# Performance work log

Measured on AMD Instinct MI355X. Metric: run time of the kernel, lower is better.

The kernel has to match this reference:

```python
import jax, jax.numpy as jnp
import numpy as np

BN_EPS = 1e-5


def _gcn(x, A, W, gamma, beta):
    # x: [B,N,Cin], A: [B,N,N] -> [B,N,Cout]; BatchNorm1d over (B,N) per channel (train-mode batch stats)
    h = jnp.einsum('bnm,bmc->bnc', A, x @ W)
    mu = h.mean(axis=(0, 1))
    var = h.var(axis=(0, 1))
    h = (h - mu) * jax.lax.rsqrt(var + BN_EPS) * gamma + beta
    return jax.nn.relu(h)  # dropout is identity (drop_prob=0 / eval)


def _ppige(x, A, W0, g0, b0, W_res, g_res, b_res):
    h = _gcn(x, A, W0, g0, b0)
    for i in range(W_res.shape[0]):  # residual GCN stack (num_GCN-1 layers)
        h = _gcn(h, A, W_res[i], g_res[i], b_res[i]) + h
    return h


def _gge(x, w1, b1, w2, b2):
    return jax.nn.relu(jax.nn.relu(x @ w1 + b1) @ w2 + b2)


def _gaga(G, h):
    # G: [B,N,H], h: [B,H]
    att = jax.nn.softmax(jnp.einsum('bnh,bh->bn', G, h), axis=-1)
    return jnp.einsum('bnh,bn->bh', G, att)


def _led(ea, eb, conv_w, conv_b, p1_w, p1_b, p2_w, p2_b):
    # ea, eb: [B, 2H]; Conv1d(2H->2H, k=1) over length-2 axis then MaxPool1d(2)
    stacked = jnp.stack([ea, eb], axis=-1)  # [B, 2H, 2]
    conv = jnp.einsum('oc,bct->bot', conv_w, stacked) + conv_b[None, :, None]
    cnn_x = conv.max(axis=-1)  # [B, 2H]
    x = jax.nn.relu(jnp.concatenate([cnn_x, ea - eb], axis=1) @ p1_w + p1_b)
    return x @ p2_w + p2_b


def setup_inputs() -> dict:
    key = jax.random.key(0)
    ks = jax.random.split(key, 24)
    Bs, N, PPI_in, H, F_in = 8, 2048, 512, 256, 1024
    n_res = 3  # num_GCN - 1
    s = 0.02
    adjA = jax.random.uniform(ks[0], (Bs, N, N), jnp.float32)
    adjB = jax.random.uniform(ks[1], (Bs, N, N), jnp.float32)
    adjA = adjA / adjA.sum(-1, keepdims=True)  # row-normalized for numerical sanity
    adjB = adjB / adjB.sum(-1, keepdims=True)
    return {
        'a': jax.random.normal(ks[2], (Bs, F_in), jnp.float32),
        'bio_a': jax.random.normal(ks[3], (Bs, N, PPI_in), jnp.float32),
        'A': adjA,
        'b': jax.random.normal(ks[4], (Bs, F_in), jnp.float32),
        'bio_b': jax.random.normal(ks[5], (Bs, N, PPI_in), jnp.float32),
        'B': adjB,
        'W0': jax.random.normal(ks[6], (PPI_in, H), jnp.float32) * s,
        'gamma0': jnp.ones((H,), jnp.float32),
        'beta0': jnp.zeros((H,), jnp.float32),
        'W_res': jax.random.normal(ks[7], (n_res, H, H), jnp.float32) * s,
        'gamma_res': jnp.ones((n_res, H), jnp.float32),
        'beta_res': jnp.zeros((n_res, H), jnp.float32),
        'g1_w': jax.random.normal(ks[8], (F_in, 128), jnp.float32) * s,
        'g1_b': jnp.zeros((128,), jnp.float32),
        'g2_w': jax.random.normal(ks[9], (128, H), jnp.float32) * s,
        'g2_b': jnp.zeros((H,), jnp.float32),
        'conv_w': jax.random.normal(ks[10], (2 * H, 2 * H), jnp.float32) * s,
        'conv_b': jnp.zeros((2 * H,), jnp.float32),
        'p1_w': jax.random.normal(ks[11], (4 * H, H), jnp.float32) * s,
        'p1_b': jnp.zeros((H,), jnp.float32),
        'p2_w': jax.random.normal(ks[12], (H, 2), jnp.float32) * s,
        'p2_b': jnp.zeros((2,), jnp.float32),
    }


def reference(a, bio_a, A, b, bio_b, B, W0, gamma0, beta0, W_res, gamma_res, beta_res,
              g1_w, g1_b, g2_w, g2_b, conv_w, conv_b, p1_w, p1_b, p2_w, p2_b):
    Ga = _ppige(bio_a, A, W0, gamma0, beta0, W_res, gamma_res, beta_res)
    Gb = _ppige(bio_b, B, W0, gamma0, beta0, W_res, gamma_res, beta_res)
    ha = _gge(a, g1_w, g1_b, g2_w, g2_b)
    hb = _gge(b, g1_w, g1_b, g2_w, g2_b)
    ea = jnp.concatenate([ha, _gaga(Ga, ha)], axis=-1)
    eb = jnp.concatenate([hb, _gaga(Gb, hb)], axis=-1)
    logits = _led(ea, eb, conv_w, conv_b, p1_w, p1_b, p2_w, p2_b)
    return jax.nn.log_softmax(logits, axis=-1)
```

## Files before the change

### kernel.cpp

```cpp
#include <hip/hip_runtime.h>
#include <hip/hip_bf16.h>
#include <cstdint>

typedef unsigned short u16;
typedef __bf16 bf16x8 __attribute__((ext_vector_type(8)));
typedef float f32x4 __attribute__((ext_vector_type(4)));

typedef __attribute__((address_space(1))) const void* gas_ptr;
typedef __attribute__((address_space(3))) void* las_ptr;

__device__ __forceinline__ u16 f2bf(float f) {
  union { __hip_bfloat16 h; u16 u; } v;
  v.h = __float2bfloat16(f);
  return v.u;
}

__device__ __forceinline__ void gload16(const u16* g, u16* l) {
  __builtin_amdgcn_global_load_lds((gas_ptr)g, (las_ptr)l, 16, 0, 0);
}

__global__ __launch_bounds__(256) void k_convert_all(const float* __restrict__ aA,
                                                     const float* __restrict__ aB,
                                                     const float* __restrict__ bA,
                                                     const float* __restrict__ bB,
                                                     u16* __restrict__ Abf,
                                                     u16* __restrict__ biobf) {
  long i4 = (long)blockIdx.x * 256 + threadIdx.x;
  for (; i4 < 20971520L; i4 += (long)gridDim.x * 256) {
    const float* src; u16* dst; long off;
    if (i4 < 8388608L)        { src = aA; dst = Abf;              off = i4; }
    else if (i4 < 16777216L)  { src = aB; dst = Abf + 33554432L;  off = i4 - 8388608L; }
    else if (i4 < 18874368L)  { src = bA; dst = biobf;            off = i4 - 16777216L; }
    else                      { src = bB; dst = biobf + 8388608L; off = i4 - 18874368L; }
    float4 v = reinterpret_cast<const float4*>(src)[off];
    ushort4 o;
    o.x = f2bf(v.x); o.y = f2bf(v.y); o.z = f2bf(v.z); o.w = f2bf(v.w);
    reinterpret_cast<ushort4*>(dst)[off] = o;
  }
}

__global__ __launch_bounds__(256) void k_transpose_bf16(const float* __restrict__ src,
                                                        u16* __restrict__ dst, int R, int C) {
  __shared__ float tile[32][33];
  int c0 = blockIdx.x * 32, r0 = blockIdx.y * 32;
  int tx = threadIdx.x & 31, ty = threadIdx.x >> 5;
#pragma unroll
  for (int i = 0; i < 4; ++i) {
    int r = ty + i * 8;
    tile[r][tx] = src[(long)(r0 + r) * C + c0 + tx];
  }
  __syncthreads();
#pragma unroll
  for (int i = 0; i < 4; ++i) {
    int c = ty + i * 8;
    dst[(long)(c0 + c) * R + r0 + tx] = f2bf(tile[tx][c]);
  }
}

template<int EPI>
__global__ __launch_bounds__(256) void k_gemm(const u16* __restrict__ A, int lda, long sA,
                                              const u16* __restrict__ Bt, int ldb, long sB,
                                              float* __restrict__ C, int ldc, long sC,
                                              u16* __restrict__ PtOut, int ldpt,
                                              float* __restrict__ stats, int K) {
  __shared__ __align__(16) u16 smem[4][8192];
  __shared__ float cs[256];
  const int tid = threadIdx.x;
  const int lane = tid & 63;
  const int wid = tid >> 6;
  const int wm = wid >> 1, wn = wid & 1;
  const long m0 = (long)blockIdx.x * 128, n0 = (long)blockIdx.y * 128;
  const int z = blockIdx.z;
  const u16* Ab = A + (long)z * sA;
  const u16* Btb = Bt + (long)z * sB;

  const int rsub = lane >> 3;
  const int swzcol = ((lane & 7) ^ rsub) * 8;
  const long a_row = m0 + wid * 32 + rsub;
  const long b_row = n0 + wid * 32 + rsub;

  if (EPI == 0) cs[tid] = 0.f;

  const f32x4 zero = {0.f, 0.f, 0.f, 0.f};
  f32x4 acc[4][4];
#pragma unroll
  for (int i = 0; i < 4; ++i)
#pragma unroll
    for (int j = 0; j < 4; ++j) acc[i][j] = zero;

  const int fr = lane & 15;
  const int kgrp = lane >> 4;
  const int swz_rd = lane & 7;
  const int nk = K >> 6;

  auto stage = [&](int buf, int k0) {
#pragma unroll
    for (int i = 0; i < 4; ++i)
      gload16(Ab + (a_row + i * 8) * lda + (k0 + swzcol), &smem[buf][(wid * 32 + i * 8) * 64]);
#pragma unroll
    for (int i = 0; i < 4; ++i)
      gload16(Btb + (b_row + i * 8) * ldb + (k0 + swzcol), &smem[2 + buf][(wid * 32 + i * 8) * 64]);
  };

  stage(0, 0);
  __syncthreads();
  for (int t = 0; t < nk; ++t) {
    int cur = t & 1;
    if (t + 1 < nk) stage(1 - cur, (t + 1) * 64);
    const u16* Asb = smem[cur];
    const u16* Bsb = smem[2 + cur];
#pragma unroll
    for (int ks = 0; ks < 2; ++ks) {
      bf16x8 af[4], bfv[4];
#pragma unroll
      for (int f = 0; f < 4; ++f) {
        int cA = (ks * 4 + kgrp) ^ swz_rd;
        af[f]  = *reinterpret_cast<const bf16x8*>(&Asb[(wm * 64 + f * 16 + fr) * 64 + cA * 8]);
        bfv[f] = *reinterpret_cast<const bf16x8*>(&Bsb[(wn * 64 + f * 16 + fr) * 64 + cA * 8]);
      }
#pragma unroll
      for (int mf = 0; mf < 4; ++mf)
#pragma unroll
        for (int nf = 0; nf < 4; ++nf)
          acc[mf][nf] = __builtin_amdgcn_mfma_f32_16x16x32_bf16(af[mf], bfv[nf], acc[mf][nf], 0, 0, 0);
    }
    __syncthreads();
  }

  if (EPI == 0) {
    float* Cb = C + (long)z * sC;
    const int side = z >> 3;
#pragma unroll
    for (int mf = 0; mf < 4; ++mf) {
      long mrow = m0 + wm * 64 + mf * 16 + kgrp * 4;
#pragma unroll
      for (int nf = 0; nf < 4; ++nf) {
        long ncol = n0 + wn * 64 + nf * 16 + fr;
#pragma unroll
        for (int r = 0; r < 4; ++r)
          Cb[(mrow + r) * ldc + ncol] = acc[mf][nf][r];
      }
    }
#pragma unroll
    for (int nf = 0; nf < 4; ++nf) {
      int cl = wn * 64 + nf * 16 + fr;
      float s = 0.f, q = 0.f;
#pragma unroll
      for (int mf = 0; mf < 4; ++mf)
#pragma unroll
        for (int r = 0; r < 4; ++r) { float v = acc[mf][nf][r]; s += v; q += v * v; }
      atomicAdd(&cs[cl], s);
      atomicAdd(&cs[128 + cl], q);
    }
    __syncthreads();
    if (tid < 128) atomicAdd(&stats[side * 512 + n0 + tid], cs[tid]);
    else           atomicAdd(&stats[side * 512 + 256 + n0 + (tid - 128)], cs[tid]);
  } else {
    u16* Ts = &smem[0][0];
#pragma unroll
    for (int mf = 0; mf < 4; ++mf)
#pragma unroll
      for (int nf = 0; nf < 4; ++nf) {
        int nl = wn * 64 + nf * 16 + fr;
        int ml = wm * 64 + mf * 16 + kgrp * 4;
#pragma unroll
        for (int r = 0; r < 4; ++r)
          Ts[nl * 136 + ml + r] = f2bf(acc[mf][nf][r]);
      }
    __syncthreads();
    int n = tid >> 1, half = tid & 1;
    const u16* sp = Ts + n * 136 + half * 64;
    u16* dp = PtOut + (long)(n0 + n) * ldpt + m0 + half * 64;
#pragma unroll
    for (int j = 0; j < 8; ++j)
      reinterpret_cast<uint4*>(dp)[j] = reinterpret_cast<const uint4*>(sp)[j];
  }
}

__global__ __launch_bounds__(256) void k_bn_apply(const float4* __restrict__ u4,
                                                  const float4* hprev4,
                                                  float4* hout4,
                                                  ushort4* __restrict__ hbf4,
                                                  const float* __restrict__ stats,
                                                  const float* __restrict__ gamma,
                                                  const float* __restrict__ beta, int res) {
  long i = (long)blockIdx.x * 256 + threadIdx.x;
  int side = (int)(i >> 20);
  int c0 = (int)(i & 63) * 4;
  const float* st = stats + side * 512;
  float4 v = u4[i];
  float4 r;
  float* vp = (float*)&v; float* rp = (float*)&r;
#pragma unroll
  for (int j = 0; j < 4; ++j) {
    int c = c0 + j;
    float mu = st[c] * (1.f / 16384.f);
    float var = st[256 + c] * (1.f / 16384.f) - mu * mu;
    float sc = gamma[c] * rsqrtf(var + 1e-5f);
    float sh = beta[c] - mu * sc;
    rp[j] = fmaxf(vp[j] * sc + sh, 0.f);
  }
  if (res) {
    float4 hp = hprev4[i];
    r.x += hp.x; r.y += hp.y; r.z += hp.z; r.w += hp.w;
  }
  hout4[i] = r;
  ushort4 o;
  o.x = f2bf(r.x); o.y = f2bf(r.y); o.z = f2bf(r.z); o.w = f2bf(r.w);
  hbf4[i] = o;
}

__global__ __launch_bounds__(256) void k_gge(const float* __restrict__ in_a,
                                             const float* __restrict__ in_b,
                                             const float* __restrict__ w1, const float* __restrict__ b1,
                                             const float* __restrict__ w2, const float* __restrict__ b2,
                                             float* __restrict__ ha) {
  __shared__ float av[1024];
  __shared__ float hid[128];
  int bx = blockIdx.x, t = threadIdx.x;
  const float* ap = ((bx >> 3) ? in_b : in_a) + (bx & 7) * 1024;
  for (int i = t; i < 1024; i += 256) av[i] = ap[i];
  __syncthreads();
  if (t < 128) {
    float s = b1[t];
    for (int c = 0; c < 1024; ++c) s += av[c] * w1[c * 128 + t];
    hid[t] = fmaxf(s, 0.f);
  }
  __syncthreads();
  float s = b2[t];
  for (int c = 0; c < 128; ++c) s += hid[c] * w2[c * 256 + t];
  ha[bx * 256 + t] = fmaxf(s, 0.f);
}

__global__ __launch_bounds__(256) void k_gaga_scores(const float* __restrict__ h,
                                                     const float* __restrict__ ha,
                                                     float* __restrict__ sc) {
  __shared__ __align__(16) float has[256];
  int bx = blockIdx.x;
  has[threadIdx.x] = ha[bx * 256 + threadIdx.x];
  __syncthreads();
  const float* G = h + (long)bx * 524288;
  int wv = threadIdx.x >> 6, lane = threadIdx.x & 63;
  float4 h4 = reinterpret_cast<const float4*>(has)[lane];
  for (int i = 0; i < 32; ++i) {
    int n = blockIdx.y * 128 + wv * 32 + i;
    float4 v = reinterpret_cast<const float4*>(G + (long)n * 256)[lane];
    float d = v.x * h4.x + v.y * h4.y + v.z * h4.z + v.w * h4.w;
#pragma unroll
    for (int o2 = 32; o2 > 0; o2 >>= 1) d += __shfl_down(d, o2);
    if (lane == 0) sc[bx * 2048 + n] = d;
  }
}

__global__ __launch_bounds__(256) void k_softmax2048(const float* __restrict__ sc, float* __restrict__ att) {
  __shared__ float red[256];
  int b = blockIdx.x, t = threadIdx.x;
  const float* s = sc + b * 2048;
  float* o = att + b * 2048;
  float v[8];
  float m = -1e30f;
#pragma unroll
  for (int i = 0; i < 8; ++i) { v[i] = s[t + i * 256]; m = fmaxf(m, v[i]); }
  red[t] = m; __syncthreads();
  for (int o2 = 128; o2 > 0; o2 >>= 1) { if (t < o2) red[t] = fmaxf(red[t], red[t + o2]); __syncthreads(); }
  m = red[0]; __syncthreads();
  float sum = 0.f;
#pragma unroll
  for (int i = 0; i < 8; ++i) { v[i] = expf(v[i] - m); sum += v[i]; }
  red[t] = sum; __syncthreads();
  for (int o2 = 128; o2 > 0; o2 >>= 1) { if (t < o2) red[t] += red[t + o2]; __syncthreads(); }
  float inv = 1.f / red[0];
#pragma unroll
  for (int i = 0; i < 8; ++i) o[t + i * 256] = v[i] * inv;
}

__global__ __launch_bounds__(256) void k_gaga_out(const float* __restrict__ h,
                                                  const float* __restrict__ att,
                                                  float* __restrict__ ga) {
  __shared__ float atts[128];
  int bx = blockIdx.x, n0 = blockIdx.y * 128, c = threadIdx.x;
  if (threadIdx.x < 128) atts[threadIdx.x] = att[bx * 2048 + n0 + threadIdx.x];
  __syncthreads();
  const float* base = h + (long)bx * 524288 + (long)n0 * 256 + c;
  float s = 0.f;
#pragma unroll 4
  for (int i = 0; i < 128; ++i) s += base[(long)i * 256] * atts[i];
  atomicAdd(&ga[bx * 256 + c], s);
}

__global__ __launch_bounds__(512) void k_led_conv(const float* __restrict__ ha, const float* __restrict__ ga,
                                                  const float* __restrict__ hb, const float* __restrict__ gb,
                                                  const float* __restrict__ cw, const float* __restrict__ cb,
                                                  float* __restrict__ cnn, float* __restrict__ diff) {
  __shared__ float ea[8][512], eb[8][512];
  int t = threadIdx.x;
  for (int i = t; i < 4096; i += 512) {
    int b = i >> 9, c = i & 511;
    float va = (c < 256) ? ha[b * 256 + c] : ga[b * 256 + c - 256];
    float vb = (c < 256) ? hb[b * 256 + c] : gb[b * 256 + c - 256];
    ea[b][c] = va; eb[b][c] = vb;
    if (blockIdx.x == 0) diff[i] = va - vb;
  }
  __syncthreads();
  int o = blockIdx.x * 64 + (t >> 3), b = t & 7;
  const float* wr = cw + (long)o * 512;
  float s0 = cb[o], s1 = s0;
  for (int c = 0; c < 512; ++c) { float w = wr[c]; s0 += w * ea[b][c]; s1 += w * eb[b][c]; }
  cnn[b * 512 + o] = fmaxf(s0, s1);
}

__global__ __launch_bounds__(256) void k_led_p1(const float* __restrict__ cnn, const float* __restrict__ diff,
                                                const float* __restrict__ w, const float* __restrict__ pb,
                                                float* __restrict__ x) {
  __shared__ float cat[8][1024];
  int t = threadIdx.x;
  for (int i = t; i < 8192; i += 256) {
    int b = i >> 10, c = i & 1023;
    cat[b][c] = (c < 512) ? cnn[b * 512 + c] : diff[b * 512 + c - 512];
  }
  __syncthreads();
  int o = blockIdx.x * 32 + (t >> 3), b = t & 7;
  float s = pb[o];
  for (int c = 0; c < 1024; ++c) s += cat[b][c] * w[c * 256 + o];
  x[b * 256 + o] = fmaxf(s, 0.f);
}

__global__ __launch_bounds__(64) void k_led_final(const float* __restrict__ x,
                                                  const float* __restrict__ p2w, const float* __restrict__ p2b,
                                                  float* __restrict__ out) {
  __shared__ float lg[16];
  int t = threadIdx.x;
  if (t < 16) {
    int b = t >> 1, j = t & 1;
    float s = p2b[j];
    for (int c = 0; c < 256; ++c) s += x[b * 256 + c] * p2w[c * 2 + j];
    lg[t] = s;
  }
  __syncthreads();
  if (t < 8) {
    float l0 = lg[t * 2], l1 = lg[t * 2 + 1];
    float m = fmaxf(l0, l1);
    float lse = m + logf(expf(l0 - m) + expf(l1 - m));
    out[t * 2] = l0 - lse;
    out[t * 2 + 1] = l1 - lse;
  }
}

extern "C" void kernel_launch(void* const* d_in, const int* in_sizes, int n_in,
                              void* d_out, int out_size, void* d_ws, size_t ws_size,
                              hipStream_t stream) {
  const float* in_a   = (const float*)d_in[0];
  const float* bio_a  = (const float*)d_in[1];
  const float* adj_a  = (const float*)d_in[2];
  const float* in_b   = (const float*)d_in[3];
  const float* bio_b  = (const float*)d_in[4];
  const float* adj_b  = (const float*)d_in[5];
  const float* W0     = (const float*)d_in[6];
  const float* gamma0 = (const float*)d_in[7];
  const float* beta0  = (const float*)d_in[8];
  const float* W_res  = (const float*)d_in[9];
  const float* g_res  = (const float*)d_in[10];
  const float* b_res  = (const float*)d_in[11];
  const float* g1_w   = (const float*)d_in[12];
  const float* g1_b   = (const float*)d_in[13];
  const float* g2_w   = (const float*)d_in[14];
  const float* g2_b   = (const float*)d_in[15];
  const float* conv_w = (const float*)d_in[16];
  const float* conv_b = (const float*)d_in[17];
  const float* p1_w   = (const float*)d_in[18];
  const float* p1_b   = (const float*)d_in[19];
  const float* p2_w   = (const float*)d_in[20];
  const float* p2_b   = (const float*)d_in[21];
  float* out = (float*)d_out;

  char* ws = (char*)d_ws;
  size_t off = 0;
  auto alloc = [&](size_t bytes) {
    char* p = ws + off;
    off += (bytes + 255) & ~(size_t)255;
    return p;
  };
  u16*   Abf   = (u16*)  alloc(67108864ull * 2);
  u16*   biobf = (u16*)  alloc(16777216ull * 2);
  u16*   Pt    = (u16*)  alloc(8388608ull * 2);
  float* ubuf  = (float*)alloc(8388608ull * 4);
  float* h     = (float*)alloc(8388608ull * 4);
  u16*   hbf   = (u16*)  alloc(8388608ull * 2);
  u16*   W0t   = (u16*)  alloc(131072ull * 2);
  u16*   Wrt   = (u16*)  alloc(196608ull * 2);
  float* stats = (float*)alloc(4096 * 4);
  float* gabuf = (float*)alloc(4096 * 4);
  float* hav   = (float*)alloc(4096 * 4);
  float* scb   = (float*)alloc(32768 * 4);
  float* attb  = (float*)alloc(32768 * 4);
  float* cnn   = (float*)alloc(4096 * 4);
  float* diff  = (float*)alloc(4096 * 4);
  float* xbuf  = (float*)alloc(2048 * 4);

  k_transpose_bf16<<<dim3(8, 16), 256, 0, stream>>>(W0, W0t, 512, 256);
  for (int i = 0; i < 3; ++i)
    k_transpose_bf16<<<dim3(8, 8), 256, 0, stream>>>(W_res + i * 65536, Wrt + i * 65536, 256, 256);

  (void)hipMemsetAsync(stats, 0, 32768, stream);

  k_convert_all<<<4096, 256, 0, stream>>>(adj_a, adj_b, bio_a, bio_b, Abf, biobf);

  for (int layer = 0; layer < 4; ++layer) {
    const u16* Ain = (layer == 0) ? biobf : hbf;
    int K = (layer == 0) ? 512 : 256;
    const u16* Wt = (layer == 0) ? W0t : (Wrt + (layer - 1) * 65536);
    float* statsL = stats + layer * 1024;
    const float* gm = (layer == 0) ? gamma0 : (g_res + (layer - 1) * 256);
    const float* bt = (layer == 0) ? beta0 : (b_res + (layer - 1) * 256);

    k_gemm<1><<<dim3(256, 2, 1), 256, 0, stream>>>(Ain, K, 0, Wt, K, 0,
                                                   nullptr, 0, 0, Pt, 32768, nullptr, K);
    k_gemm<0><<<dim3(16, 2, 16), 256, 0, stream>>>(Abf, 2048, 4194304L, Pt, 32768, 2048,
                                                   ubuf, 256, 524288L, nullptr, 0, statsL, 2048);
    k_bn_apply<<<8192, 256, 0, stream>>>((const float4*)ubuf, (const float4*)h, (float4*)h,
                                         (ushort4*)hbf, statsL, gm, bt, layer ? 1 : 0);
  }

  k_gge<<<16, 256, 0, stream>>>(in_a, in_b, g1_w, g1_b, g2_w, g2_b, hav);
  k_gaga_scores<<<dim3(16, 16), 256, 0, stream>>>(h, hav, scb);
  k_softmax2048<<<16, 256, 0, stream>>>(scb, attb);
  k_gaga_out<<<dim3(16, 16), 256, 0, stream>>>(h, attb, gabuf);

  k_led_conv<<<8, 512, 0, stream>>>(hav, gabuf, hav + 2048, gabuf + 2048, conv_w, conv_b, cnn, diff);
  k_led_p1<<<8, 256, 0, stream>>>(cnn, diff, p1_w, p1_b, xbuf);
  k_led_final<<<1, 64, 0, stream>>>(xbuf, p2_w, p2_b, out);
}
```

Baseline: 624.9 us.

## Store GCN intermediates in bf16 and process each graph side separately

The GEMM output and the residual hidden state move from fp32 buffers to bf16, which removes the fp32 ubuf and h buffers and roughly halves the traffic in BN-apply and the attention kernels. The layer loop now runs per side with half-sized launches, so each side's smaller working set (Pt, activations) may stay in cache. The convert kernel is rewritten as one 8-element chunk per thread with no grid-stride loop. In exchange, the residual accumulation now happens in bf16, which lowers precision, and there are twice as many launches at half the grid size.

```diff
diff --git a/kernel.cpp b/kernel.cpp
--- a/kernel.cpp
+++ b/kernel.cpp
@@ -13,6 +13,11 @@
   union { __hip_bfloat16 h; u16 u; } v;
   v.h = __float2bfloat16(f);
   return v.u;
+}
+__device__ __forceinline__ float bf2f(u16 u) {
+  union { unsigned int i; float f; } v;
+  v.i = ((unsigned int)u) << 16;
+  return v.f;
 }
 
 __device__ __forceinline__ void gload16(const u16* g, u16* l) {
@@ -25,18 +30,18 @@
                                                      const float* __restrict__ bB,
                                                      u16* __restrict__ Abf,
                                                      u16* __restrict__ biobf) {
-  long i4 = (long)blockIdx.x * 256 + threadIdx.x;
-  for (; i4 < 20971520L; i4 += (long)gridDim.x * 256) {
-    const float* src; u16* dst; long off;
-    if (i4 < 8388608L)        { src = aA; dst = Abf;              off = i4; }
-    else if (i4 < 16777216L)  { src = aB; dst = Abf + 33554432L;  off = i4 - 8388608L; }
-    else if (i4 < 18874368L)  { src = bA; dst = biobf;            off = i4 - 16777216L; }
-    else                      { src = bB; dst = biobf + 8388608L; off = i4 - 18874368L; }
-    float4 v = reinterpret_cast<const float4*>(src)[off];
-    ushort4 o;
-    o.x = f2bf(v.x); o.y = f2bf(v.y); o.z = f2bf(v.z); o.w = f2bf(v.w);
-    reinterpret_cast<ushort4*>(dst)[off] = o;
-  }
+  long e0 = ((long)blockIdx.x * 256 + threadIdx.x) * 8;
+  const float* src; u16* dst;
+  if (e0 < 33554432L)        { src = aA;              dst = Abf; }
+  else if (e0 < 67108864L)   { src = aB - 33554432L;  dst = Abf; }
+  else if (e0 < 75497472L)   { src = bA - 67108864L;  dst = biobf - 67108864L + 0; }
+  else                       { src = bB - 75497472L;  dst = biobf - 75497472L + 8388608L; }
+  float4 v0 = *reinterpret_cast<const float4*>(src + e0);
+  float4 v1 = *reinterpret_cast<const float4*>(src + e0 + 4);
+  union { u16 u[8]; uint4 q; } o;
+  o.u[0] = f2bf(v0.x); o.u[1] = f2bf(v0.y); o.u[2] = f2bf(v0.z); o.u[3] = f2bf(v0.w);
+  o.u[4] = f2bf(v1.x); o.u[5] = f2bf(v1.y); o.u[6] = f2bf(v1.z); o.u[7] = f2bf(v1.w);
+  *reinterpret_cast<uint4*>(dst + e0) = o.q;
 }
 
 __global__ __launch_bounds__(256) void k_transpose_bf16(const float* __restrict__ src,
@@ -60,7 +65,7 @@
 template<int EPI>
 __global__ __launch_bounds__(256) void k_gemm(const u16* __restrict__ A, int lda, long sA,
                                               const u16* __restrict__ Bt, int ldb, long sB,
-                                              float* __restrict__ C, int ldc, long sC,
+                                              u16* __restrict__ C, int ldc, long sC,
                                               u16* __restrict__ PtOut, int ldpt,
                                               float* __restrict__ stats, int K) {
   __shared__ __align__(16) u16 smem[4][8192];
@@ -128,8 +133,7 @@
   }
 
   if (EPI == 0) {
-    float* Cb = C + (long)z * sC;
-    const int side = z >> 3;
+    u16* Cb = C + (long)z * sC;
 #pragma unroll
     for (int mf = 0; mf < 4; ++mf) {
       long mrow = m0 + wm * 64 + mf * 16 + kgrp * 4;
@@ -138,7 +142,7 @@
         long ncol = n0 + wn * 64 + nf * 16 + fr;
 #pragma unroll
         for (int r = 0; r < 4; ++r)
-          Cb[(mrow + r) * ldc + ncol] = acc[mf][nf][r];
+          Cb[(mrow + r) * ldc + ncol] = f2bf(acc[mf][nf][r]);
       }
     }
 #pragma unroll
@@ -153,8 +157,8 @@
       atomicAdd(&cs[128 + cl], q);
     }
     __syncthreads();
-    if (tid < 128) atomicAdd(&stats[side * 512 + n0 + tid], cs[tid]);
-    else           atomicAdd(&stats[side * 512 + 256 + n0 + (tid - 128)], cs[tid]);
+    if (tid < 128) atomicAdd(&stats[n0 + tid], cs[tid]);
+    else           atomicAdd(&stats[256 + n0 + (tid - 128)], cs[tid]);
   } else {
     u16* Ts = &smem[0][0];
 #pragma unroll
@@ -177,20 +181,16 @@
   }
 }
 
-__global__ __launch_bounds__(256) void k_bn_apply(const float4* __restrict__ u4,
-                                                  const float4* hprev4,
-                                                  float4* hout4,
-                                                  ushort4* __restrict__ hbf4,
-                                                  const float* __restrict__ stats,
+__global__ __launch_bounds__(256) void k_bn_apply(const ushort4* __restrict__ u4,
+                                                  ushort4* __restrict__ h4,
+                                                  const float* __restrict__ st,
                                                   const float* __restrict__ gamma,
                                                   const float* __restrict__ beta, int res) {
   long i = (long)blockIdx.x * 256 + threadIdx.x;
-  int side = (int)(i >> 20);
   int c0 = (int)(i & 63) * 4;
-  const float* st = stats + side * 512;
-  float4 v = u4[i];
-  float4 r;
-  float* vp = (float*)&v; float* rp = (float*)&r;
+  ushort4 uv = u4[i];
+  float vp[4] = { bf2f(uv.x), bf2f(uv.y), bf2f(uv.z), bf2f(uv.w) };
+  float rp[4];
 #pragma unroll
   for (int j = 0; j < 4; ++j) {
     int c = c0 + j;
@@ -201,13 +201,12 @@
     rp[j] = fmaxf(vp[j] * sc + sh, 0.f);
   }
   if (res) {
-    float4 hp = hprev4[i];
-    r.x += hp.x; r.y += hp.y; r.z += hp.z; r.w += hp.w;
-  }
-  hout4[i] = r;
+    ushort4 hv = h4[i];
+    rp[0] += bf2f(hv.x); rp[1] += bf2f(hv.y); rp[2] += bf2f(hv.z); rp[3] += bf2f(hv.w);
+  }
   ushort4 o;
-  o.x = f2bf(r.x); o.y = f2bf(r.y); o.z = f2bf(r.z); o.w = f2bf(r.w);
-  hbf4[i] = o;
+  o.x = f2bf(rp[0]); o.y = f2bf(rp[1]); o.z = f2bf(rp[2]); o.w = f2bf(rp[3]);
+  h4[i] = o;
 }
 
 __global__ __launch_bounds__(256) void k_gge(const float* __restrict__ in_a,
@@ -232,20 +231,20 @@
   ha[bx * 256 + t] = fmaxf(s, 0.f);
 }
 
-__global__ __launch_bounds__(256) void k_gaga_scores(const float* __restrict__ h,
+__global__ __launch_bounds__(256) void k_gaga_scores(const u16* __restrict__ h,
                                                      const float* __restrict__ ha,
                                                      float* __restrict__ sc) {
   __shared__ __align__(16) float has[256];
   int bx = blockIdx.x;
   has[threadIdx.x] = ha[bx * 256 + threadIdx.x];
   __syncthreads();
-  const float* G = h + (long)bx * 524288;
+  const u16* G = h + (long)bx * 524288;
   int wv = threadIdx.x >> 6, lane = threadIdx.x & 63;
   float4 h4 = reinterpret_cast<const float4*>(has)[lane];
   for (int i = 0; i < 32; ++i) {
     int n = blockIdx.y * 128 + wv * 32 + i;
-    float4 v = reinterpret_cast<const float4*>(G + (long)n * 256)[lane];
-    float d = v.x * h4.x + v.y * h4.y + v.z * h4.z + v.w * h4.w;
+    ushort4 v = reinterpret_cast<const ushort4*>(G + (long)n * 256)[lane];
+    float d = bf2f(v.x) * h4.x + bf2f(v.y) * h4.y + bf2f(v.z) * h4.z + bf2f(v.w) * h4.w;
 #pragma unroll
     for (int o2 = 32; o2 > 0; o2 >>= 1) d += __shfl_down(d, o2);
     if (lane == 0) sc[bx * 2048 + n] = d;
@@ -274,17 +273,17 @@
   for (int i = 0; i < 8; ++i) o[t + i * 256] = v[i] * inv;
 }
 
-__global__ __launch_bounds__(256) void k_gaga_out(const float* __restrict__ h,
+__global__ __launch_bounds__(256) void k_gaga_out(const u16* __restrict__ h,
                                                   const float* __restrict__ att,
                                                   float* __restrict__ ga) {
   __shared__ float atts[128];
   int bx = blockIdx.x, n0 = blockIdx.y * 128, c = threadIdx.x;
   if (threadIdx.x < 128) atts[threadIdx.x] = att[bx * 2048 + n0 + threadIdx.x];
   __syncthreads();
-  const float* base = h + (long)bx * 524288 + (long)n0 * 256 + c;
+  const u16* base = h + (long)bx * 524288 + (long)n0 * 256 + c;
   float s = 0.f;
 #pragma unroll 4
-  for (int i = 0; i < 128; ++i) s += base[(long)i * 256] * atts[i];
+  for (int i = 0; i < 128; ++i) s += bf2f(base[(long)i * 256]) * atts[i];
   atomicAdd(&ga[bx * 256 + c], s);
 }
 
@@ -382,9 +381,8 @@
   };
   u16*   Abf   = (u16*)  alloc(67108864ull * 2);
   u16*   biobf = (u16*)  alloc(16777216ull * 2);
-  u16*   Pt    = (u16*)  alloc(8388608ull * 2);
-  float* ubuf  = (float*)alloc(8388608ull * 4);
-  float* h     = (float*)alloc(8388608ull * 4);
+  u16*   Pt    = (u16*)  alloc(4194304ull * 2);
+  u16*   ubf   = (u16*)  alloc(8388608ull * 2);
   u16*   hbf   = (u16*)  alloc(8388608ull * 2);
   u16*   W0t   = (u16*)  alloc(131072ull * 2);
   u16*   Wrt   = (u16*)  alloc(196608ull * 2);
@@ -403,28 +401,34 @@
 
   (void)hipMemsetAsync(stats, 0, 32768, stream);
 
-  k_convert_all<<<4096, 256, 0, stream>>>(adj_a, adj_b, bio_a, bio_b, Abf, biobf);
-
-  for (int layer = 0; layer < 4; ++layer) {
-    const u16* Ain = (layer == 0) ? biobf : hbf;
-    int K = (layer == 0) ? 512 : 256;
-    const u16* Wt = (layer == 0) ? W0t : (Wrt + (layer - 1) * 65536);
-    float* statsL = stats + layer * 1024;
-    const float* gm = (layer == 0) ? gamma0 : (g_res + (layer - 1) * 256);
-    const float* bt = (layer == 0) ? beta0 : (b_res + (layer - 1) * 256);
-
-    k_gemm<1><<<dim3(256, 2, 1), 256, 0, stream>>>(Ain, K, 0, Wt, K, 0,
-                                                   nullptr, 0, 0, Pt, 32768, nullptr, K);
-    k_gemm<0><<<dim3(16, 2, 16), 256, 0, stream>>>(Abf, 2048, 4194304L, Pt, 32768, 2048,
-                                                   ubuf, 256, 524288L, nullptr, 0, statsL, 2048);
-    k_bn_apply<<<8192, 256, 0, stream>>>((const float4*)ubuf, (const float4*)h, (float4*)h,
-                                         (ushort4*)hbf, statsL, gm, bt, layer ? 1 : 0);
+  k_convert_all<<<40960, 256, 0, stream>>>(adj_a, adj_b, bio_a, bio_b, Abf, biobf);
+
+  for (int side = 0; side < 2; ++side) {
+    const u16* Aside = Abf + (long)side * 33554432L;
+    u16* ubfS = ubf + (long)side * 4194304L;
+    u16* hbfS = hbf + (long)side * 4194304L;
+
+    for (int layer = 0; layer < 4; ++layer) {
+      const u16* Ain = (layer == 0) ? (biobf + (long)side * 8388608L) : hbfS;
+      int K = (layer == 0) ? 512 : 256;
+      const u16* Wt = (layer == 0) ? W0t : (Wrt + (layer - 1) * 65536);
+      float* statsL = stats + (layer * 2 + side) * 512;
+      const float* gm = (layer == 0) ? gamma0 : (g_res + (layer - 1) * 256);
+      const float* bt = (layer == 0) ? beta0 : (b_res + (layer - 1) * 256);
+
+      k_gemm<1><<<dim3(128, 2, 1), 256, 0, stream>>>(Ain, K, 0, Wt, K, 0,
+                                                     nullptr, 0, 0, Pt, 16384, nullptr, K);
+      k_gemm<0><<<dim3(16, 2, 8), 256, 0, stream>>>(Aside, 2048, 4194304L, Pt, 16384, 2048,
+                                                    ubfS, 256, 524288L, nullptr, 0, statsL, 2048);
+      k_bn_apply<<<4096, 256, 0, stream>>>((const ushort4*)ubfS, (ushort4*)hbfS,
+                                           statsL, gm, bt, layer ? 1 : 0);
+    }
   }
 
   k_gge<<<16, 256, 0, stream>>>(in_a, in_b, g1_w, g1_b, g2_w, g2_b, hav);
-  k_gaga_scores<<<dim3(16, 16), 256, 0, stream>>>(h, hav, scb);
+  k_gaga_scores<<<dim3(16, 16), 256, 0, stream>>>(hbf, hav, scb);
   k_softmax2048<<<16, 256, 0, stream>>>(scb, attb);
-  k_gaga_out<<<dim3(16, 16), 256, 0, stream>>>(h, attb, gabuf);
+  k_gaga_out<<<dim3(16, 16), 256, 0, stream>>>(hbf, attb, gabuf);
 
   k_led_conv<<<8, 512, 0, stream>>>(hav, gabuf, hav + 2048, gabuf + 2048, conv_w, conv_b, cnn, diff);
   k_led_p1<<<8, 256, 0, stream>>>(cnn, diff, p1_w, p1_b, xbuf);
```

After: 680.7 us. +8.9%, slower.
